# Kernel optimization log

Hardware: AMD Instinct MI355X
Metric: run time of the kernel (lower is better)

Reference implementation:

```python
import jax, jax.numpy as jnp
import numpy as np

# ---- static config (mirrors GridEncoder.__init__ kwargs) ----
INPUT_DIM = 3
NUM_LEVELS = 3          # CUDA wrapper hardcodes L = 3
LEVEL_DIM = 2           # C
PER_LEVEL_SCALE = 2.0
BASE_RESOLUTION = 128   # H
LOG2_HASHMAP_SIZE = 19
ALIGN_CORNERS = False
INTERP_ID = 0           # 0 = linear, 1 = smoothstep
B = 2097152             # number of query points
PLANE_H, PLANE_W = 1024, 512  # 3*PLANE_H*PLANE_W == offsets[-1]
PRIMES = (1, 2654435761, 805459861)  # instant-NGP spatial hash primes
S = float(np.log2(PER_LEVEL_SCALE))


def _compute_offsets():
    # replicates GridEncoder.__init__ offset construction
    offsets, offset = [], 0
    max_params = 2 ** LOG2_HASHMAP_SIZE
    for i in range(NUM_LEVELS):
        resolution = int(np.ceil(BASE_RESOLUTION * PER_LEVEL_SCALE ** i))
        params = min(max_params, (resolution if ALIGN_CORNERS else resolution + 1) ** INPUT_DIM)
        params = int(np.ceil(params / 8) * 8)
        offsets.append(offset)
        offset += params
    offsets.append(offset)
    return offsets


def setup_inputs() -> dict:
    key = jax.random.key(0)
    k1, k2 = jax.random.split(key)
    total = _compute_offsets()[-1]
    assert 3 * PLANE_H * PLANE_W == total, (total,)
    # learned triplane feature maps (embeddings.normal_(0, 0.1) in reset_parameters)
    triplane = 0.1 * jax.random.normal(k1, (3, LEVEL_DIM, PLANE_H, PLANE_W), dtype=jnp.float32)
    # query coordinates in [-bound, bound] = [-1, 1]
    inputs = jax.random.uniform(k2, (B, INPUT_DIM), dtype=jnp.float32, minval=-1.0, maxval=1.0)
    return {"triplane": triplane, "inputs": inputs}


def _grid_encode(x01, embeddings):
    # x01: [B, D] in [0,1]; embeddings: [offsets[-1], C] flat multi-level table
    offsets = _compute_offsets()
    D, C = INPUT_DIM, LEVEL_DIM
    n_corners = 2 ** D
    # binary corner offsets [8, 3]
    corners = jnp.array([[(i >> d) & 1 for d in range(D)] for i in range(n_corners)],
                        dtype=jnp.uint32)
    out = jnp.zeros((x01.shape[0], C), dtype=embeddings.dtype)
    for level in range(NUM_LEVELS):
        scale = 2.0 ** (level * S) * BASE_RESOLUTION - 1.0
        res = int(np.ceil(scale)) + 1
        hmap = offsets[level + 1] - offsets[level]
        pos = x01 * scale + (0.0 if ALIGN_CORNERS else 0.5)
        pos_grid = jnp.floor(pos)
        frac = pos - pos_grid                      # [B, D] in [0,1)
        if INTERP_ID == 1:  # smoothstep
            frac = frac * frac * (3.0 - 2.0 * frac)
        pg = pos_grid.astype(jnp.uint32)
        cp = pg[:, None, :] + corners[None, :, :]  # [B, 8, D] corner coords
        stride_dim = res if ALIGN_CORNERS else res + 1
        if stride_dim ** D > hmap:  # hash indexing (uint32 mult wraps, as in CUDA)
            p = jnp.array(PRIMES, dtype=jnp.uint32)
            h = cp * p
            idx = h[..., 0] ^ h[..., 1] ^ h[..., 2]
        else:  # dense (tiled) indexing
            strides = jnp.array([stride_dim ** d for d in range(D)], dtype=jnp.uint32)
            idx = jnp.sum(cp * strides, axis=-1, dtype=jnp.uint32)
        idx = (idx % jnp.uint32(hmap)).astype(jnp.int32) + offsets[level]  # [B, 8]
        feats = embeddings[idx]                    # [B, 8, C] gather
        # trilinear weights: prod over dims of frac / (1-frac) per corner bit
        w = jnp.prod(jnp.where(corners[None].astype(bool),
                               frac[:, None, :], 1.0 - frac[:, None, :]), axis=-1)  # [B, 8]
        out = out + jnp.einsum('bk,bkc->bc', w, feats)
    return out


def reference(triplane, inputs):
    bound = 1.0
    x01 = (inputs + bound) / (2.0 * bound)  # map to [0, 1]
    # triplane_.squeeze().permute(0,2,3,1).reshape(-1, level_dim)
    emb = jnp.transpose(triplane, (0, 2, 3, 1)).reshape(-1, LEVEL_DIM)
    return _grid_encode(x01, emb)  # [B, C]
```

## Files before the change

### kernel.cpp

```cpp
#include <hip/hip_runtime.h>
#include <hip/hip_fp16.h>


#define NPOINTS  2097152
#define HMASK    0x7FFFFu
#define PLANE    524288
#define NTAB     (3 * PLANE)
#define GBLOCKS  2048
#define TTHREADS (GBLOCKS * 256)
#define PPT      4

typedef float    floatx2 __attribute__((ext_vector_type(2)));
typedef unsigned uintx2  __attribute__((ext_vector_type(2)));
typedef unsigned uintx4  __attribute__((ext_vector_type(4)));

__device__ __forceinline__ unsigned pack2(float a, float b) {
    const __half2 h2 = __halves2half2(__float2half_rn(a), __float2half_rn(b));
    return *reinterpret_cast<const unsigned*>(&h2);
}

__global__ __launch_bounds__(256) void tp_convert_kernel(
    const float* __restrict__ tp, uintx4* __restrict__ tbl)
{
    const unsigned t = blockIdx.x * 256u + threadIdx.x;
    const unsigned level = t >> 17;
    const unsigned i4    = (t & 131071u) << 2;
    const float* __restrict__ b = tp + level * (2u * PLANE);
    const float4 c0 = *reinterpret_cast<const float4*>(b + i4);
    const float4 c1 = *reinterpret_cast<const float4*>(b + PLANE + i4);
    uintx4 o;
    o.x = pack2(c0.x, c1.x);
    o.y = pack2(c0.y, c1.y);
    o.z = pack2(c0.z, c1.z);
    o.w = pack2(c0.w, c1.w);
    tbl[t] = o;
}

__device__ __forceinline__ unsigned sel4(uintx4 q, unsigned o) {
    const unsigned a = (o & 1u) ? q.y : q.x;
    const unsigned b = (o & 1u) ? q.w : q.z;
    return (o & 2u) ? b : a;
}

__global__ __launch_bounds__(256) void grid_gather_kernel(
    const unsigned* __restrict__ tbl,
    const float* __restrict__ inputs,
    floatx2* __restrict__ out)
{
    const int t = blockIdx.x * 256 + threadIdx.x;

    float x0[PPT], y0[PPT], z0[PPT];
#pragma unroll
    for (int p = 0; p < PPT; ++p) {
        const int i = t + p * TTHREADS;
        const float x = __builtin_nontemporal_load(&inputs[3 * i + 0]);
        const float y = __builtin_nontemporal_load(&inputs[3 * i + 1]);
        const float z = __builtin_nontemporal_load(&inputs[3 * i + 2]);
        x0[p] = (x + 1.0f) * 0.5f;
        y0[p] = (y + 1.0f) * 0.5f;
        z0[p] = (z + 1.0f) * 0.5f;
    }

    float o0[PPT], o1[PPT];
#pragma unroll
    for (int p = 0; p < PPT; ++p) { o0[p] = 0.0f; o1[p] = 0.0f; }

#pragma unroll
    for (int level = 0; level < 3; ++level) {
        const float scale = (float)((128 << level) - 1);
        const unsigned lvl = (unsigned)level << 19;

#pragma unroll
        for (int p = 0; p < PPT; ++p) {
            const float px = fmaf(x0[p], scale, 0.5f);
            const float py = fmaf(y0[p], scale, 0.5f);
            const float pz = fmaf(z0[p], scale, 0.5f);
            const float fx = floorf(px), fy = floorf(py), fz = floorf(pz);
            const float rx = px - fx, ry = py - fy, rz = pz - fz;
            const unsigned gx = (unsigned)fx, gy = (unsigned)fy, gz = (unsigned)fz;

            const unsigned d = gx ^ (gx + 1u);
            const unsigned hy0 = gy * 2654435761u;
            const unsigned hy1 = (gy + 1u) * 2654435761u;
            const unsigned hz0 = gz * 805459861u;
            const unsigned hz1 = (gz + 1u) * 805459861u;

            unsigned P0[4];
            P0[0] = lvl | ((gx ^ hy0 ^ hz0) & HMASK);
            P0[1] = lvl | ((gx ^ hy1 ^ hz0) & HMASK);
            P0[2] = lvl | ((gx ^ hy0 ^ hz1) & HMASK);
            P0[3] = lvl | ((gx ^ hy1 ^ hz1) & HMASK);

            unsigned e0[4], e1[4];
            if (d == 1u) {
#pragma unroll
                for (int j = 0; j < 4; ++j) {
                    const unsigned P = P0[j];
                    const uintx2 q = *reinterpret_cast<const uintx2*>(tbl + (P & ~1u));
                    const unsigned o = P & 1u;
                    e0[j] = o ? q.y : q.x;
                    e1[j] = o ? q.x : q.y;
                }
            } else if (d == 3u) {
#pragma unroll
                for (int j = 0; j < 4; ++j) {
                    const unsigned P = P0[j];
                    const uintx4 q = *reinterpret_cast<const uintx4*>(tbl + (P & ~3u));
                    const unsigned o = P & 3u;
                    e0[j] = sel4(q, o);
                    e1[j] = sel4(q, o ^ 3u);
                }
            } else {
#pragma unroll
                for (int j = 0; j < 4; ++j) {
                    const unsigned P = P0[j];
                    e0[j] = tbl[P];
                    e1[j] = tbl[P ^ d];
                }
            }

            const float wx1 = rx, wx0 = 1.0f - rx;
            const float wy1 = ry, wy0 = 1.0f - ry;
            const float wz1 = rz, wz0 = 1.0f - rz;
            const float wyz[4] = { wy0 * wz0, wy1 * wz0, wy0 * wz1, wy1 * wz1 };
#pragma unroll
            for (int j = 0; j < 4; ++j) {
                const __half2 a = *reinterpret_cast<const __half2*>(&e0[j]);
                const __half2 b = *reinterpret_cast<const __half2*>(&e1[j]);
                const float2 fa = __half22float2(a);
                const float2 fb = __half22float2(b);
                const float wA = wx0 * wyz[j], wB = wx1 * wyz[j];
                o0[p] = fmaf(wA, fa.x, o0[p]); o1[p] = fmaf(wA, fa.y, o1[p]);
                o0[p] = fmaf(wB, fb.x, o0[p]); o1[p] = fmaf(wB, fb.y, o1[p]);
            }
        }
        __syncthreads();
    }

#pragma unroll
    for (int p = 0; p < PPT; ++p) {
        floatx2 r; r.x = o0[p]; r.y = o1[p];
        __builtin_nontemporal_store(r, &out[t + p * TTHREADS]);
    }
}

__global__ __launch_bounds__(256) void grid_fallback_kernel(
    const float* __restrict__ triplane,
    const float* __restrict__ inputs,
    float* __restrict__ out)
{
    const int i = blockIdx.x * blockDim.x + threadIdx.x;
    if (i >= NPOINTS) return;
    const float x0 = (inputs[3 * i + 0] + 1.0f) * 0.5f;
    const float y0 = (inputs[3 * i + 1] + 1.0f) * 0.5f;
    const float z0 = (inputs[3 * i + 2] + 1.0f) * 0.5f;
    float o0 = 0.0f, o1 = 0.0f;
#pragma unroll
    for (int level = 0; level < 3; ++level) {
        const float scale = (float)((128 << level) - 1);
        const float px = fmaf(x0, scale, 0.5f);
        const float py = fmaf(y0, scale, 0.5f);
        const float pz = fmaf(z0, scale, 0.5f);
        const float fx = floorf(px), fy = floorf(py), fz = floorf(pz);
        const float rx = px - fx, ry = py - fy, rz = pz - fz;
        const unsigned gx = (unsigned)fx, gy = (unsigned)fy, gz = (unsigned)fz;
        const float* __restrict__ base = triplane + level * (2 * PLANE);
#pragma unroll
        for (int c = 0; c < 8; ++c) {
            const unsigned bx = (c >> 0) & 1, by = (c >> 1) & 1, bz = (c >> 2) & 1;
            const unsigned h = (gx + bx) ^ ((gy + by) * 2654435761u) ^ ((gz + bz) * 805459861u);
            const unsigned local = h & HMASK;
            const float w = (bx ? rx : 1.0f - rx) * (by ? ry : 1.0f - ry) * (bz ? rz : 1.0f - rz);
            o0 = fmaf(w, base[local], o0);
            o1 = fmaf(w, base[PLANE + local], o1);
        }
    }
    reinterpret_cast<float2*>(out)[i] = make_float2(o0, o1);
}

extern "C" void kernel_launch(void* const* d_in, const int* in_sizes, int n_in,
                              void* d_out, int out_size, void* d_ws, size_t ws_size,
                              hipStream_t stream) {
    const float* triplane = (const float*)d_in[0];
    const float* inputs   = (const float*)d_in[1];
    const int threads = 256;

    if (ws_size >= (size_t)NTAB * sizeof(unsigned)) {
        unsigned* tbl = (unsigned*)d_ws;
        tp_convert_kernel<<<(NTAB / 4) / threads, threads, 0, stream>>>(
            triplane, (uintx4*)tbl);
        grid_gather_kernel<<<GBLOCKS, threads, 0, stream>>>(tbl, inputs, (floatx2*)d_out);
    } else {
        grid_fallback_kernel<<<NPOINTS / threads, threads, 0, stream>>>(
            triplane, inputs, (float*)d_out);
    }
}
```

Baseline: 197.6 us.

## Unify gather into 16-byte loads, double points per thread, nontemporal convert loads

The gather kernel now always issues a 16-byte aligned load per y/z corner pair and takes the x-neighbour from that vector when it falls in the same 4-entry group, issuing a separate scalar load only otherwise. This removes the three-way branch on the x-neighbour distance, which diverged across lanes. Points per thread go from 4 to 8 with half the blocks, and launch bounds now request 4 waves per SIMD. The convert kernel switches to nontemporal vector loads. The trade-offs are more register pressure, fewer blocks in flight, and wider loads that may fetch unused data.

```diff
diff --git a/kernel.cpp b/kernel.cpp
--- a/kernel.cpp
+++ b/kernel.cpp
@@ -6,11 +6,12 @@
 #define HMASK    0x7FFFFu
 #define PLANE    524288
 #define NTAB     (3 * PLANE)
-#define GBLOCKS  2048
+#define GBLOCKS  1024
 #define TTHREADS (GBLOCKS * 256)
-#define PPT      4
+#define PPT      8
 
 typedef float    floatx2 __attribute__((ext_vector_type(2)));
+typedef float    floatx4 __attribute__((ext_vector_type(4)));
 typedef unsigned uintx2  __attribute__((ext_vector_type(2)));
 typedef unsigned uintx4  __attribute__((ext_vector_type(4)));
 
@@ -26,8 +27,10 @@
     const unsigned level = t >> 17;
     const unsigned i4    = (t & 131071u) << 2;
     const float* __restrict__ b = tp + level * (2u * PLANE);
-    const float4 c0 = *reinterpret_cast<const float4*>(b + i4);
-    const float4 c1 = *reinterpret_cast<const float4*>(b + PLANE + i4);
+    const floatx4 c0 = __builtin_nontemporal_load(
+        reinterpret_cast<const floatx4*>(b + i4));
+    const floatx4 c1 = __builtin_nontemporal_load(
+        reinterpret_cast<const floatx4*>(b + PLANE + i4));
     uintx4 o;
     o.x = pack2(c0.x, c1.x);
     o.y = pack2(c0.y, c1.y);
@@ -42,7 +45,7 @@
     return (o & 2u) ? b : a;
 }
 
-__global__ __launch_bounds__(256) void grid_gather_kernel(
+__global__ __launch_bounds__(256, 4) void grid_gather_kernel(
     const unsigned* __restrict__ tbl,
     const float* __restrict__ inputs,
     floatx2* __restrict__ out)
@@ -85,48 +88,36 @@
             const unsigned hz0 = gz * 805459861u;
             const unsigned hz1 = (gz + 1u) * 805459861u;
 
-            unsigned P0[4];
-            P0[0] = lvl | ((gx ^ hy0 ^ hz0) & HMASK);
-            P0[1] = lvl | ((gx ^ hy1 ^ hz0) & HMASK);
-            P0[2] = lvl | ((gx ^ hy0 ^ hz1) & HMASK);
-            P0[3] = lvl | ((gx ^ hy1 ^ hz1) & HMASK);
+            unsigned P[4];
+            P[0] = lvl | ((gx ^ hy0 ^ hz0) & HMASK);
+            P[1] = lvl | ((gx ^ hy1 ^ hz0) & HMASK);
+            P[2] = lvl | ((gx ^ hy0 ^ hz1) & HMASK);
+            P[3] = lvl | ((gx ^ hy1 ^ hz1) & HMASK);
 
-            unsigned e0[4], e1[4];
-            if (d == 1u) {
+            uintx4 q[4];
 #pragma unroll
-                for (int j = 0; j < 4; ++j) {
-                    const unsigned P = P0[j];
-                    const uintx2 q = *reinterpret_cast<const uintx2*>(tbl + (P & ~1u));
-                    const unsigned o = P & 1u;
-                    e0[j] = o ? q.y : q.x;
-                    e1[j] = o ? q.x : q.y;
-                }
-            } else if (d == 3u) {
-#pragma unroll
-                for (int j = 0; j < 4; ++j) {
-                    const unsigned P = P0[j];
-                    const uintx4 q = *reinterpret_cast<const uintx4*>(tbl + (P & ~3u));
-                    const unsigned o = P & 3u;
-                    e0[j] = sel4(q, o);
-                    e1[j] = sel4(q, o ^ 3u);
-                }
-            } else {
-#pragma unroll
-                for (int j = 0; j < 4; ++j) {
-                    const unsigned P = P0[j];
-                    e0[j] = tbl[P];
-                    e1[j] = tbl[P ^ d];
-                }
-            }
+            for (int j = 0; j < 4; ++j)
+                q[j] = *reinterpret_cast<const uintx4*>(tbl + (P[j] & ~3u));
 
             const float wx1 = rx, wx0 = 1.0f - rx;
             const float wy1 = ry, wy0 = 1.0f - ry;
             const float wz1 = rz, wz0 = 1.0f - rz;
             const float wyz[4] = { wy0 * wz0, wy1 * wz0, wy0 * wz1, wy1 * wz1 };
+
+            unsigned e1v[4];
+            if (d > 3u) {
+#pragma unroll
+                for (int j = 0; j < 4; ++j) e1v[j] = tbl[P[j] ^ d];
+            } else {
+#pragma unroll
+                for (int j = 0; j < 4; ++j) e1v[j] = sel4(q[j], (P[j] & 3u) ^ d);
+            }
+
 #pragma unroll
             for (int j = 0; j < 4; ++j) {
-                const __half2 a = *reinterpret_cast<const __half2*>(&e0[j]);
-                const __half2 b = *reinterpret_cast<const __half2*>(&e1[j]);
+                const unsigned e0 = sel4(q[j], P[j] & 3u);
+                const __half2 a = *reinterpret_cast<const __half2*>(&e0);
+                const __half2 b = *reinterpret_cast<const __half2*>(&e1v[j]);
                 const float2 fa = __half22float2(a);
                 const float2 fb = __half22float2(b);
                 const float wA = wx0 * wyz[j], wB = wx1 * wyz[j];
```

Result: slower. 624.4 us (+215.9%).
